# Performance work log

Hardware: AMD Instinct MI355X
Metric: run time of the kernel (lower is better)

## Reference

```python
import jax, jax.numpy as jnp
import numpy as np

TANH_CONST = 2.5
TEMPERATURE = 5.0


def setup_inputs() -> dict:
    key = jax.random.key(0)
    ks = jax.random.split(key, 9)
    B, L, NB, H, NC = 16384, 64, 8, 128, 1000
    return {
        "class_ids": jax.random.randint(ks[0], (B,), 0, NC),
        "gumbel_u": jax.random.uniform(ks[1], (L, B, NB), dtype=jnp.float32),
        "g_emb": jax.random.normal(ks[2], (NC, H), dtype=jnp.float32) * 0.1,
        "w_emb": jax.random.normal(ks[3], (NB, H), dtype=jnp.float32) * 0.1,
        "w_soft": jax.random.normal(ks[4], (NB, H), dtype=jnp.float32) * 0.1,
        "w_ih": jax.random.normal(ks[5], (4 * H, H), dtype=jnp.float32) * 0.1,
        "w_hh": jax.random.normal(ks[6], (4 * H, H), dtype=jnp.float32) * 0.1,
        "b_ih": jax.random.normal(ks[7], (4 * H,), dtype=jnp.float32) * 0.1,
        "b_hh": jax.random.normal(ks[8], (4 * H,), dtype=jnp.float32) * 0.1,
    }


def reference(class_ids, gumbel_u, g_emb, w_emb, w_soft, w_ih, w_hh, b_ih, b_hh):
    B = class_ids.shape[0]
    H = g_emb.shape[1]
    x0 = g_emb[class_ids]                      # [B, H] class embedding (reused each step)
    h0 = jnp.zeros((B, H), x0.dtype)
    c0 = jnp.zeros((B, H), x0.dtype)

    def step(carry, u):
        h, c, x = carry
        gates = x @ w_ih.T + h @ w_hh.T + b_ih + b_hh   # [B, 4H], torch gate order i,f,g,o
        i, f, g, o = jnp.split(gates, 4, axis=-1)
        c2 = jax.nn.sigmoid(f) * c + jax.nn.sigmoid(i) * jnp.tanh(g)
        h2 = jax.nn.sigmoid(o) * jnp.tanh(c2)
        logit = h2 @ w_soft.T                           # [B, NB]
        logit = TANH_CONST * jnp.tanh(logit / TEMPERATURE)
        # categorical sample via gumbel-max
        uc = jnp.clip(u, 1e-8, 1.0 - 1e-8)
        gmb = -jnp.log(-jnp.log(uc))
        branch = jnp.argmax(logit + gmb, axis=-1)       # [B] int
        logp = jax.nn.log_softmax(logit, axis=-1)
        lp = jnp.take_along_axis(logp, branch[:, None], axis=1)[:, 0]
        ent = -jnp.sum(jnp.exp(logp) * logp, axis=-1)
        x2 = (w_emb[branch] + x0) * 0.5
        return (h2, c2, x2), (branch, lp, ent)

    _, (arcs, lps, ents) = jax.lax.scan(step, (h0, c0, x0), gumbel_u)
    # stack along dim=1 like torch.stack(..., dim=1) -> [B, L]
    sample_arc = arcs.T
    sample_log_prob = lps.T
    sample_entropy = ents.T
    sample_prob = jnp.exp(sample_log_prob)
    return sample_arc, sample_log_prob, sample_entropy, sample_prob
```

## Files before the change

### kernel.cpp

```cpp
#include <hip/hip_runtime.h>
#include <math.h>

#define HD 128
#define NBR 8
#define LSTEPS 64
#define TILE_B 32
#define HT_PAD 36
#define PART_PAD 65

#define WHH2_OFF  0
#define WIH2_OFF  65536
#define PP_OFF    131072
#define BS_OFF    135168

__device__ __forceinline__ float fsig(float x) {
  return __builtin_amdgcn_rcpf(1.f + __expf(-x));
}
__device__ __forceinline__ float ftanh(float x) {
  return 1.f - 2.f * __builtin_amdgcn_rcpf(1.f + __expf(2.f * x));
}

__global__ __launch_bounds__(256) void setup_kernel(
    const float* __restrict__ w_emb, const float* __restrict__ w_ih,
    const float* __restrict__ w_hh, const float* __restrict__ b_ih,
    const float* __restrict__ b_hh, float* __restrict__ ws)
{
  int tid = blockIdx.x * blockDim.x + threadIdx.x;
  if (tid < 65536) {
    int hh = tid >> 9, k = (tid >> 2) & 127, q = tid & 3;
    ws[WHH2_OFF + tid] = w_hh[(q*HD + hh)*HD + k];
    ws[WIH2_OFF + tid] = w_ih[(q*HD + hh)*HD + k];
  }
  if (tid < 4096) {
    int j = tid >> 9, rem = tid & 511;
    int hh2 = rem >> 2, q = rem & 3;
    const float* wr = w_ih + (q*HD + hh2)*HD;
    const float* er = w_emb + j*HD;
    float s = 0.f;
    for (int k = 0; k < HD; ++k) s = fmaf(er[k], wr[k], s);
    ws[PP_OFF + tid] = 0.5f * s;
  }
  if (tid < 512) ws[BS_OFF + tid] = b_ih[tid] + b_hh[tid];
}

__global__ __launch_bounds__(256, 2) void ctrl_kernel(
    const int* __restrict__ class_ids,
    const float* __restrict__ gumbel_u,
    const float* __restrict__ g_emb,
    const float* __restrict__ w_soft,
    const float* __restrict__ ws,
    float* __restrict__ out,
    int Btot)
{
  __shared__ float hT[HD * HT_PAD];
  __shared__ float ws_l[NBR * HD];
  __shared__ float pp_l[NBR * HD * 4];
  __shared__ float part_l[TILE_B * PART_PAD];
  __shared__ int   br_l[TILE_B];

  const int tid = threadIdx.x;
  const int b0  = blockIdx.x * TILE_B;
  const size_t BL = (size_t)Btot * LSTEPS;

  for (int i = tid; i < NBR*HD; i += 256) ws_l[i] = w_soft[i];
  for (int i = tid; i < NBR*HD*4; i += 256) pp_l[i] = ws[PP_OFF + i];

  const int hh = tid & 127;
  const int bg = tid >> 7;

  float bsq[4];
  #pragma unroll
  for (int q = 0; q < 4; ++q) bsq[q] = ws[BS_OFF + q*HD + hh];

  const float* __restrict__ whhp = ws + WHH2_OFF + hh*512;
  const float* __restrict__ wihp = ws + WIH2_OFF + hh*512;
  const float* hTb = hT + bg*16;

  {
    int sb = tid >> 3;
    int kc = tid & 7;
    int cid = class_ids[b0 + sb];
    const float* src = g_emb + (size_t)cid * HD + kc*16;
    #pragma unroll
    for (int ii = 0; ii < 4; ++ii) {
      float4 v = *(const float4*)(src + 4*ii);
      int kb = kc*16 + 4*ii;
      hT[(kb+0)*HT_PAD + sb] = v.x;
      hT[(kb+1)*HT_PAD + sb] = v.y;
      hT[(kb+2)*HT_PAD + sb] = v.z;
      hT[(kb+3)*HT_PAD + sb] = v.w;
    }
  }
  __syncthreads();

  float q0[4][16];
  #pragma unroll
  for (int q = 0; q < 4; ++q)
    #pragma unroll
    for (int j = 0; j < 16; ++j) q0[q][j] = 0.f;

  #pragma unroll 8
  for (int k = 0; k < HD; ++k) {
    float4 w = *(const float4*)(wihp + k*4);
    const float* hr = hTb + k*HT_PAD;
    float4 h0 = *(const float4*)(hr);
    float4 h1 = *(const float4*)(hr+4);
    float4 h2 = *(const float4*)(hr+8);
    float4 h3 = *(const float4*)(hr+12);
    #pragma unroll
    for (int q = 0; q < 4; ++q) {
      float wq = (q==0)?w.x:((q==1)?w.y:((q==2)?w.z:w.w));
      q0[q][0]=fmaf(h0.x,wq,q0[q][0]); q0[q][1]=fmaf(h0.y,wq,q0[q][1]);
      q0[q][2]=fmaf(h0.z,wq,q0[q][2]); q0[q][3]=fmaf(h0.w,wq,q0[q][3]);
      q0[q][4]=fmaf(h1.x,wq,q0[q][4]); q0[q][5]=fmaf(h1.y,wq,q0[q][5]);
      q0[q][6]=fmaf(h1.z,wq,q0[q][6]); q0[q][7]=fmaf(h1.w,wq,q0[q][7]);
      q0[q][8]=fmaf(h2.x,wq,q0[q][8]); q0[q][9]=fmaf(h2.y,wq,q0[q][9]);
      q0[q][10]=fmaf(h2.z,wq,q0[q][10]); q0[q][11]=fmaf(h2.w,wq,q0[q][11]);
      q0[q][12]=fmaf(h3.x,wq,q0[q][12]); q0[q][13]=fmaf(h3.y,wq,q0[q][13]);
      q0[q][14]=fmaf(h3.z,wq,q0[q][14]); q0[q][15]=fmaf(h3.w,wq,q0[q][15]);
    }
  }
  __syncthreads();

  float c[16];
  #pragma unroll
  for (int j = 0; j < 16; ++j) c[j] = 0.f;

  for (int t = 0; t < LSTEPS; ++t) {
    float4 ua = make_float4(0,0,0,0), ub = make_float4(0,0,0,0);
    if (tid < TILE_B) {
      const float* up = gumbel_u + ((size_t)t * Btot + (b0 + tid)) * NBR;
      ua = *(const float4*)up;
      ub = *(const float4*)(up + 4);
    }

    float h2v[16];

    if (t == 0) {
      #pragma unroll
      for (int j = 0; j < 16; ++j) {
        float gi = q0[0][j] + bsq[0];
        float gf = q0[1][j] + bsq[1];
        float gg = q0[2][j] + bsq[2];
        float go = q0[3][j] + bsq[3];
        float c2 = fsig(gf)*c[j] + fsig(gi)*ftanh(gg);
        c[j] = c2;
        h2v[j] = fsig(go) * ftanh(c2);
      }
      #pragma unroll
      for (int q = 0; q < 4; ++q)
        #pragma unroll
        for (int j = 0; j < 16; ++j) q0[q][j] = fmaf(q0[q][j], 0.5f, bsq[q]);
    } else {
      float acc[4][16];
      #pragma unroll
      for (int q = 0; q < 4; ++q)
        #pragma unroll
        for (int j = 0; j < 16; ++j) acc[q][j] = 0.f;

      #pragma unroll 8
      for (int k = 0; k < HD; ++k) {
        float4 w = *(const float4*)(whhp + k*4);
        const float* hr = hTb + k*HT_PAD;
        float4 h0 = *(const float4*)(hr);
        float4 h1 = *(const float4*)(hr+4);
        float4 h2 = *(const float4*)(hr+8);
        float4 h3 = *(const float4*)(hr+12);
        #pragma unroll
        for (int q = 0; q < 4; ++q) {
          float wq = (q==0)?w.x:((q==1)?w.y:((q==2)?w.z:w.w));
          acc[q][0]=fmaf(h0.x,wq,acc[q][0]); acc[q][1]=fmaf(h0.y,wq,acc[q][1]);
          acc[q][2]=fmaf(h0.z,wq,acc[q][2]); acc[q][3]=fmaf(h0.w,wq,acc[q][3]);
          acc[q][4]=fmaf(h1.x,wq,acc[q][4]); acc[q][5]=fmaf(h1.y,wq,acc[q][5]);
          acc[q][6]=fmaf(h1.z,wq,acc[q][6]); acc[q][7]=fmaf(h1.w,wq,acc[q][7]);
          acc[q][8]=fmaf(h2.x,wq,acc[q][8]); acc[q][9]=fmaf(h2.y,wq,acc[q][9]);
          acc[q][10]=fmaf(h2.z,wq,acc[q][10]); acc[q][11]=fmaf(h2.w,wq,acc[q][11]);
          acc[q][12]=fmaf(h3.x,wq,acc[q][12]); acc[q][13]=fmaf(h3.y,wq,acc[q][13]);
          acc[q][14]=fmaf(h3.z,wq,acc[q][14]); acc[q][15]=fmaf(h3.w,wq,acc[q][15]);
        }
      }

      #pragma unroll
      for (int j = 0; j < 16; ++j) {
        int br = br_l[bg*16 + j];
        float4 pv = *(const float4*)(&pp_l[(br*HD + hh)*4]);
        float gi = (acc[0][j] + q0[0][j]) + pv.x;
        float gf = (acc[1][j] + q0[1][j]) + pv.y;
        float gg = (acc[2][j] + q0[2][j]) + pv.z;
        float go = (acc[3][j] + q0[3][j]) + pv.w;
        float c2 = fsig(gf)*c[j] + fsig(gi)*ftanh(gg);
        c[j] = c2;
        h2v[j] = fsig(go) * ftanh(c2);
      }
    }
    __syncthreads();

    {
      float* dst = &hT[hh*HT_PAD + bg*16];
      *(float4*)(dst)    = make_float4(h2v[0],h2v[1],h2v[2],h2v[3]);
      *(float4*)(dst+4)  = make_float4(h2v[4],h2v[5],h2v[6],h2v[7]);
      *(float4*)(dst+8)  = make_float4(h2v[8],h2v[9],h2v[10],h2v[11]);
      *(float4*)(dst+12) = make_float4(h2v[12],h2v[13],h2v[14],h2v[15]);
    }
    __syncthreads();

    {
      int lb = tid & 31, ch = tid >> 5;
      float part[8];
      #pragma unroll
      for (int nb = 0; nb < 8; ++nb) part[nb] = 0.f;
      #pragma unroll
      for (int i = 0; i < 16; ++i) {
        float hvv = hT[(ch*16 + i)*HT_PAD + lb];
        #pragma unroll
        for (int nb = 0; nb < 8; ++nb)
          part[nb] = fmaf(hvv, ws_l[nb*HD + ch*16 + i], part[nb]);
      }
      #pragma unroll
      for (int nb = 0; nb < 8; ++nb)
        part_l[lb*PART_PAD + nb*8 + ch] = part[nb];
    }
    __syncthreads();

    if (tid < TILE_B) {
      int lb = tid;
      float lg[8];
      #pragma unroll
      for (int nb = 0; nb < 8; ++nb) {
        float s = 0.f;
        #pragma unroll
        for (int ch = 0; ch < 8; ++ch) s += part_l[lb*PART_PAD + nb*8 + ch];
        lg[nb] = 2.5f * ftanh(s * 0.2f);
      }
      float uv[8] = {ua.x,ua.y,ua.z,ua.w,ub.x,ub.y,ub.z,ub.w};
      int br = 0; float best;
      {
        float uc = fminf(fmaxf(uv[0], 1e-8f), 0.99999999f);
        best = lg[0] - __logf(-__logf(uc));
      }
      #pragma unroll
      for (int nb = 1; nb < 8; ++nb) {
        float uc = fminf(fmaxf(uv[nb], 1e-8f), 0.99999999f);
        float y = lg[nb] - __logf(-__logf(uc));
        if (y > best) { best = y; br = nb; }
      }
      float m = lg[0];
      #pragma unroll
      for (int nb = 1; nb < 8; ++nb) m = fmaxf(m, lg[nb]);
      float se = 0.f;
      #pragma unroll
      for (int nb = 0; nb < 8; ++nb) se += __expf(lg[nb] - m);
      float lse = __logf(se);
      float lp = (lg[br] - m) - lse;
      float ent = 0.f;
      #pragma unroll
      for (int nb = 0; nb < 8; ++nb) {
        float lpi = (lg[nb] - m) - lse;
        ent -= __expf(lpi) * lpi;
      }
      size_t row = (size_t)(b0 + lb) * LSTEPS + t;
      out[row]        = (float)br;
      out[BL + row]   = lp;
      out[2*BL + row] = ent;
      out[3*BL + row] = __expf(lp);
      br_l[lb] = br;
    }
    __syncthreads();
  }
}

extern "C" void kernel_launch(void* const* d_in, const int* in_sizes, int n_in,
                              void* d_out, int out_size, void* d_ws, size_t ws_size,
                              hipStream_t stream) {
  const int*   class_ids = (const int*)d_in[0];
  const float* gumbel_u  = (const float*)d_in[1];
  const float* g_emb     = (const float*)d_in[2];
  const float* w_emb     = (const float*)d_in[3];
  const float* w_soft    = (const float*)d_in[4];
  const float* w_ih      = (const float*)d_in[5];
  const float* w_hh      = (const float*)d_in[6];
  const float* b_ih      = (const float*)d_in[7];
  const float* b_hh      = (const float*)d_in[8];
  float* out = (float*)d_out;
  float* ws  = (float*)d_ws;
  int B = in_sizes[0];

  hipLaunchKernelGGL(setup_kernel, dim3(256), dim3(256), 0, stream,
                     w_emb, w_ih, w_hh, b_ih, b_hh, ws);
  hipLaunchKernelGGL(ctrl_kernel, dim3(B / TILE_B), dim3(256), 0, stream,
                     class_ids, gumbel_u, g_emb, w_soft, ws, out, B);
}
```

Measured before the change: 2.225 ms.

## Precompute per-class input projections and restructure LSTM recurrence to 128-thread blocks

Adds a setup pass that computes the class-embedding input projection (plus bias) for every class, so the main kernel looks up a per-class row instead of running a per-block x0 GEMM. The recurrent GEMM is remapped so 128 threads each own 8 gate columns (two hidden units, all four gates) for 16 batch rows, with h written straight to shared memory. This removes one barrier and the extra register transpose, and the gate weights now come from global/L2 instead of LDS. The risk is heavier register pressure (16x8 accumulators), lower thread-level parallelism per block, and extra setup work proportional to the number of classes.

```diff
diff --git a/kernel.cpp b/kernel.cpp
--- a/kernel.cpp
+++ b/kernel.cpp
@@ -6,12 +6,12 @@
 #define LSTEPS 64
 #define TILE_B 32
 #define HT_PAD 36
-#define PART_PAD 65
-
-#define WHH2_OFF  0
-#define WIH2_OFF  65536
-#define PP_OFF    131072
-#define BS_OFF    135168
+#define PART_PAD 33
+
+#define QB_OFF   0
+#define WHH_OFF  524288
+#define PP_OFF   589824
+#define B2_OFF   593920
 
 __device__ __forceinline__ float fsig(float x) {
   return __builtin_amdgcn_rcpf(1.f + __expf(-x));
@@ -21,32 +21,54 @@
 }
 
 __global__ __launch_bounds__(256) void setup_kernel(
-    const float* __restrict__ w_emb, const float* __restrict__ w_ih,
-    const float* __restrict__ w_hh, const float* __restrict__ b_ih,
-    const float* __restrict__ b_hh, float* __restrict__ ws)
+    const float* __restrict__ g_emb, const float* __restrict__ w_emb,
+    const float* __restrict__ w_ih,  const float* __restrict__ w_hh,
+    const float* __restrict__ b_ih,  const float* __restrict__ b_hh,
+    float* __restrict__ ws, int NC)
 {
-  int tid = blockIdx.x * blockDim.x + threadIdx.x;
-  if (tid < 65536) {
-    int hh = tid >> 9, k = (tid >> 2) & 127, q = tid & 3;
-    ws[WHH2_OFF + tid] = w_hh[(q*HD + hh)*HD + k];
-    ws[WIH2_OFF + tid] = w_ih[(q*HD + hh)*HD + k];
-  }
-  if (tid < 4096) {
-    int j = tid >> 9, rem = tid & 511;
-    int hh2 = rem >> 2, q = rem & 3;
-    const float* wr = w_ih + (q*HD + hh2)*HD;
-    const float* er = w_emb + j*HD;
+  int tid = blockIdx.x * 256 + threadIdx.x;
+  int qbN = NC * 512;
+  if (tid < qbN) {
+    int cls = tid >> 9, col = tid & 511;
+    int cg = col >> 3, hid = (col >> 2) & 1, q = col & 3;
+    int row = q*HD + 2*cg + hid;
+    const float* er = g_emb + (size_t)cls * HD;
+    const float* wr = w_ih + (size_t)row * HD;
     float s = 0.f;
     for (int k = 0; k < HD; ++k) s = fmaf(er[k], wr[k], s);
-    ws[PP_OFF + tid] = 0.5f * s;
-  }
-  if (tid < 512) ws[BS_OFF + tid] = b_ih[tid] + b_hh[tid];
-}
-
-__global__ __launch_bounds__(256, 2) void ctrl_kernel(
+    ws[QB_OFF + tid] = 0.5f * s + b_ih[row] + b_hh[row];
+    return;
+  }
+  int t2 = tid - qbN;
+  if (t2 < 65536) {
+    int k = t2 >> 9, col = t2 & 511;
+    int cg = col >> 3, hid = (col >> 2) & 1, q = col & 3;
+    ws[WHH_OFF + t2] = w_hh[(q*HD + 2*cg + hid)*HD + k];
+    return;
+  }
+  int t3 = t2 - 65536;
+  if (t3 < 4096) {
+    int br = t3 >> 9, col = t3 & 511;
+    int cg = col >> 3, hid = (col >> 2) & 1, q = col & 3;
+    int row = q*HD + 2*cg + hid;
+    const float* er = w_emb + br*HD;
+    const float* wr = w_ih + (size_t)row * HD;
+    float s = 0.f;
+    for (int k = 0; k < HD; ++k) s = fmaf(er[k], wr[k], s);
+    ws[PP_OFF + t3] = 0.5f * s;
+    return;
+  }
+  int t4 = t3 - 4096;
+  if (t4 < 512) {
+    int cg = t4 >> 3, hid = (t4 >> 2) & 1, q = t4 & 3;
+    int row = q*HD + 2*cg + hid;
+    ws[B2_OFF + t4] = b_ih[row] + b_hh[row];
+  }
+}
+
+__global__ __launch_bounds__(128, 1) void ctrl_kernel(
     const int* __restrict__ class_ids,
     const float* __restrict__ gumbel_u,
-    const float* __restrict__ g_emb,
     const float* __restrict__ w_soft,
     const float* __restrict__ ws,
     float* __restrict__ out,
@@ -54,77 +76,41 @@
 {
   __shared__ float hT[HD * HT_PAD];
   __shared__ float ws_l[NBR * HD];
-  __shared__ float pp_l[NBR * HD * 4];
   __shared__ float part_l[TILE_B * PART_PAD];
   __shared__ int   br_l[TILE_B];
 
   const int tid = threadIdx.x;
+  const int cg  = tid & 63;
+  const int bg  = tid >> 6;
   const int b0  = blockIdx.x * TILE_B;
   const size_t BL = (size_t)Btot * LSTEPS;
 
-  for (int i = tid; i < NBR*HD; i += 256) ws_l[i] = w_soft[i];
-  for (int i = tid; i < NBR*HD*4; i += 256) pp_l[i] = ws[PP_OFF + i];
-
-  const int hh = tid & 127;
-  const int bg = tid >> 7;
-
-  float bsq[4];
+  for (int i = tid; i < NBR*HD; i += 128) ws_l[i] = w_soft[i];
+
+  const float* __restrict__ wkbase = ws + WHH_OFF + cg*8;
+  const float* __restrict__ qb     = ws + QB_OFF + cg*8;
+  const float* __restrict__ ppb    = ws + PP_OFF + cg*8;
+
+  float bias8[8];
+  {
+    const float* bp = ws + B2_OFF + cg*8;
+    float4 bA = *(const float4*)(bp);
+    float4 bB = *(const float4*)(bp + 4);
+    bias8[0]=bA.x; bias8[1]=bA.y; bias8[2]=bA.z; bias8[3]=bA.w;
+    bias8[4]=bB.x; bias8[5]=bB.y; bias8[6]=bB.z; bias8[7]=bB.w;
+  }
+
+  int cidq[16];
   #pragma unroll
-  for (int q = 0; q < 4; ++q) bsq[q] = ws[BS_OFF + q*HD + hh];
-
-  const float* __restrict__ whhp = ws + WHH2_OFF + hh*512;
-  const float* __restrict__ wihp = ws + WIH2_OFF + hh*512;
-  const float* hTb = hT + bg*16;
-
-  {
-    int sb = tid >> 3;
-    int kc = tid & 7;
-    int cid = class_ids[b0 + sb];
-    const float* src = g_emb + (size_t)cid * HD + kc*16;
-    #pragma unroll
-    for (int ii = 0; ii < 4; ++ii) {
-      float4 v = *(const float4*)(src + 4*ii);
-      int kb = kc*16 + 4*ii;
-      hT[(kb+0)*HT_PAD + sb] = v.x;
-      hT[(kb+1)*HT_PAD + sb] = v.y;
-      hT[(kb+2)*HT_PAD + sb] = v.z;
-      hT[(kb+3)*HT_PAD + sb] = v.w;
-    }
-  }
-  __syncthreads();
-
-  float q0[4][16];
+  for (int j = 0; j < 16; ++j)
+    cidq[j] = class_ids[b0 + bg*16 + j] << 9;
+
+  float cc[16][2];
   #pragma unroll
-  for (int q = 0; q < 4; ++q)
-    #pragma unroll
-    for (int j = 0; j < 16; ++j) q0[q][j] = 0.f;
-
-  #pragma unroll 8
-  for (int k = 0; k < HD; ++k) {
-    float4 w = *(const float4*)(wihp + k*4);
-    const float* hr = hTb + k*HT_PAD;
-    float4 h0 = *(const float4*)(hr);
-    float4 h1 = *(const float4*)(hr+4);
-    float4 h2 = *(const float4*)(hr+8);
-    float4 h3 = *(const float4*)(hr+12);
-    #pragma unroll
-    for (int q = 0; q < 4; ++q) {
-      float wq = (q==0)?w.x:((q==1)?w.y:((q==2)?w.z:w.w));
-      q0[q][0]=fmaf(h0.x,wq,q0[q][0]); q0[q][1]=fmaf(h0.y,wq,q0[q][1]);
-      q0[q][2]=fmaf(h0.z,wq,q0[q][2]); q0[q][3]=fmaf(h0.w,wq,q0[q][3]);
-      q0[q][4]=fmaf(h1.x,wq,q0[q][4]); q0[q][5]=fmaf(h1.y,wq,q0[q][5]);
-      q0[q][6]=fmaf(h1.z,wq,q0[q][6]); q0[q][7]=fmaf(h1.w,wq,q0[q][7]);
-      q0[q][8]=fmaf(h2.x,wq,q0[q][8]); q0[q][9]=fmaf(h2.y,wq,q0[q][9]);
-      q0[q][10]=fmaf(h2.z,wq,q0[q][10]); q0[q][11]=fmaf(h2.w,wq,q0[q][11]);
-      q0[q][12]=fmaf(h3.x,wq,q0[q][12]); q0[q][13]=fmaf(h3.y,wq,q0[q][13]);
-      q0[q][14]=fmaf(h3.z,wq,q0[q][14]); q0[q][15]=fmaf(h3.w,wq,q0[q][15]);
-    }
-  }
-  __syncthreads();
-
-  float c[16];
-  #pragma unroll
-  for (int j = 0; j < 16; ++j) c[j] = 0.f;
+  for (int j = 0; j < 16; ++j) { cc[j][0] = 0.f; cc[j][1] = 0.f; }
+
+  const int s_lb = tid & 31;
+  const int s_ch = tid >> 5;
 
   for (int t = 0; t < LSTEPS; ++t) {
     float4 ua = make_float4(0,0,0,0), ub = make_float4(0,0,0,0);
@@ -134,91 +120,96 @@
       ub = *(const float4*)(up + 4);
     }
 
-    float h2v[16];
-
-    if (t == 0) {
-      #pragma unroll
-      for (int j = 0; j < 16; ++j) {
-        float gi = q0[0][j] + bsq[0];
-        float gf = q0[1][j] + bsq[1];
-        float gg = q0[2][j] + bsq[2];
-        float go = q0[3][j] + bsq[3];
-        float c2 = fsig(gf)*c[j] + fsig(gi)*ftanh(gg);
-        c[j] = c2;
-        h2v[j] = fsig(go) * ftanh(c2);
-      }
-      #pragma unroll
-      for (int q = 0; q < 4; ++q)
+    float acc[16][8];
+    #pragma unroll
+    for (int j = 0; j < 16; ++j)
+      #pragma unroll
+      for (int g = 0; g < 8; ++g) acc[j][g] = 0.f;
+
+    if (t > 0) {
+      const float* wk = wkbase;
+      const float* hr = &hT[bg*16];
+      #pragma unroll 2
+      for (int k = 0; k < HD; ++k) {
+        float4 w0 = *(const float4*)(wk);
+        float4 w1 = *(const float4*)(wk + 4);
+        wk += 512;
+        float4 h0 = *(const float4*)(hr);
+        float4 h1 = *(const float4*)(hr + 4);
+        float4 h2 = *(const float4*)(hr + 8);
+        float4 h3 = *(const float4*)(hr + 12);
+        hr += HT_PAD;
+        #define FMAJ(j, hv) \
+          acc[j][0]=fmaf(hv,w0.x,acc[j][0]); acc[j][1]=fmaf(hv,w0.y,acc[j][1]); \
+          acc[j][2]=fmaf(hv,w0.z,acc[j][2]); acc[j][3]=fmaf(hv,w0.w,acc[j][3]); \
+          acc[j][4]=fmaf(hv,w1.x,acc[j][4]); acc[j][5]=fmaf(hv,w1.y,acc[j][5]); \
+          acc[j][6]=fmaf(hv,w1.z,acc[j][6]); acc[j][7]=fmaf(hv,w1.w,acc[j][7]);
+        FMAJ(0,  h0.x) FMAJ(1,  h0.y) FMAJ(2,  h0.z) FMAJ(3,  h0.w)
+        FMAJ(4,  h1.x) FMAJ(5,  h1.y) FMAJ(6,  h1.z) FMAJ(7,  h1.w)
+        FMAJ(8,  h2.x) FMAJ(9,  h2.y) FMAJ(10, h2.z) FMAJ(11, h2.w)
+        FMAJ(12, h3.x) FMAJ(13, h3.y) FMAJ(14, h3.z) FMAJ(15, h3.w)
+        #undef FMAJ
+      }
+    }
+    __syncthreads();
+
+    #pragma unroll
+    for (int j = 0; j < 16; ++j) {
+      int jb = bg*16 + j;
+      const float* qrow = qb + cidq[j];
+      float4 qv0 = *(const float4*)(qrow);
+      float4 qv1 = *(const float4*)(qrow + 4);
+      float4 pv0, pv1;
+      if (t == 0) {
+        pv0.x = qv0.x - bias8[0]; pv0.y = qv0.y - bias8[1];
+        pv0.z = qv0.z - bias8[2]; pv0.w = qv0.w - bias8[3];
+        pv1.x = qv1.x - bias8[4]; pv1.y = qv1.y - bias8[5];
+        pv1.z = qv1.z - bias8[6]; pv1.w = qv1.w - bias8[7];
+      } else {
+        const float* prow = ppb + (br_l[jb] << 9);
+        pv0 = *(const float4*)(prow);
+        pv1 = *(const float4*)(prow + 4);
+      }
+      float gi = acc[j][0] + qv0.x + pv0.x;
+      float gf = acc[j][1] + qv0.y + pv0.y;
+      float gc = acc[j][2] + qv0.z + pv0.z;
+      float go = acc[j][3] + qv0.w + pv0.w;
+      float c0 = fsig(gf)*cc[j][0] + fsig(gi)*ftanh(gc);
+      cc[j][0] = c0;
+      hT[(2*cg)*HT_PAD + jb] = fsig(go)*ftanh(c0);
+      gi = acc[j][4] + qv1.x + pv1.x;
+      gf = acc[j][5] + qv1.y + pv1.y;
+      gc = acc[j][6] + qv1.z + pv1.z;
+      go = acc[j][7] + qv1.w + pv1.w;
+      float c1 = fsig(gf)*cc[j][1] + fsig(gi)*ftanh(gc);
+      cc[j][1] = c1;
+      hT[(2*cg+1)*HT_PAD + jb] = fsig(go)*ftanh(c1);
+    }
+    __syncthreads();
+
+    {
+      const float* hcol = &hT[(s_ch*32)*HT_PAD + s_lb];
+      float part[8];
+      #pragma unroll
+      for (int nb = 0; nb < 8; ++nb) part[nb] = 0.f;
+      #pragma unroll
+      for (int ii = 0; ii < 32; ii += 4) {
+        float hv0 = hcol[(ii+0)*HT_PAD];
+        float hv1 = hcol[(ii+1)*HT_PAD];
+        float hv2 = hcol[(ii+2)*HT_PAD];
+        float hv3 = hcol[(ii+3)*HT_PAD];
         #pragma unroll
-        for (int j = 0; j < 16; ++j) q0[q][j] = fmaf(q0[q][j], 0.5f, bsq[q]);
-    } else {
-      float acc[4][16];
-      #pragma unroll
-      for (int q = 0; q < 4; ++q)
-        #pragma unroll
-        for (int j = 0; j < 16; ++j) acc[q][j] = 0.f;
-
-      #pragma unroll 8
-      for (int k = 0; k < HD; ++k) {
-        float4 w = *(const float4*)(whhp + k*4);
-        const float* hr = hTb + k*HT_PAD;
-        float4 h0 = *(const float4*)(hr);
-        float4 h1 = *(const float4*)(hr+4);
-        float4 h2 = *(const float4*)(hr+8);
-        float4 h3 = *(const float4*)(hr+12);
-        #pragma unroll
-        for (int q = 0; q < 4; ++q) {
-          float wq = (q==0)?w.x:((q==1)?w.y:((q==2)?w.z:w.w));
-          acc[q][0]=fmaf(h0.x,wq,acc[q][0]); acc[q][1]=fmaf(h0.y,wq,acc[q][1]);
-          acc[q][2]=fmaf(h0.z,wq,acc[q][2]); acc[q][3]=fmaf(h0.w,wq,acc[q][3]);
-          acc[q][4]=fmaf(h1.x,wq,acc[q][4]); acc[q][5]=fmaf(h1.y,wq,acc[q][5]);
-          acc[q][6]=fmaf(h1.z,wq,acc[q][6]); acc[q][7]=fmaf(h1.w,wq,acc[q][7]);
-          acc[q][8]=fmaf(h2.x,wq,acc[q][8]); acc[q][9]=fmaf(h2.y,wq,acc[q][9]);
-          acc[q][10]=fmaf(h2.z,wq,acc[q][10]); acc[q][11]=fmaf(h2.w,wq,acc[q][11]);
-          acc[q][12]=fmaf(h3.x,wq,acc[q][12]); acc[q][13]=fmaf(h3.y,wq,acc[q][13]);
-          acc[q][14]=fmaf(h3.z,wq,acc[q][14]); acc[q][15]=fmaf(h3.w,wq,acc[q][15]);
+        for (int nb = 0; nb < 8; ++nb) {
+          float4 wv = *(const float4*)(&ws_l[nb*HD + s_ch*32 + ii]);
+          part[nb] = fmaf(hv0, wv.x, part[nb]);
+          part[nb] = fmaf(hv1, wv.y, part[nb]);
+          part[nb] = fmaf(hv2, wv.z, part[nb]);
+          part[nb] = fmaf(hv3, wv.w, part[nb]);
         }
       }
-
-      #pragma unroll
-      for (int j = 0; j < 16; ++j) {
-        int br = br_l[bg*16 + j];
-        float4 pv = *(const float4*)(&pp_l[(br*HD + hh)*4]);
-        float gi = (acc[0][j] + q0[0][j]) + pv.x;
-        float gf = (acc[1][j] + q0[1][j]) + pv.y;
-        float gg = (acc[2][j] + q0[2][j]) + pv.z;
-        float go = (acc[3][j] + q0[3][j]) + pv.w;
-        float c2 = fsig(gf)*c[j] + fsig(gi)*ftanh(gg);
-        c[j] = c2;
-        h2v[j] = fsig(go) * ftanh(c2);
-      }
-    }
-    __syncthreads();
-
-    {
-      float* dst = &hT[hh*HT_PAD + bg*16];
-      *(float4*)(dst)    = make_float4(h2v[0],h2v[1],h2v[2],h2v[3]);
-      *(float4*)(dst+4)  = make_float4(h2v[4],h2v[5],h2v[6],h2v[7]);
-      *(float4*)(dst+8)  = make_float4(h2v[8],h2v[9],h2v[10],h2v[11]);
-      *(float4*)(dst+12) = make_float4(h2v[12],h2v[13],h2v[14],h2v[15]);
-    }
-    __syncthreads();
-
-    {
-      int lb = tid & 31, ch = tid >> 5;
-      float part[8];
-      #pragma unroll
-      for (int nb = 0; nb < 8; ++nb) part[nb] = 0.f;
-      #pragma unroll
-      for (int i = 0; i < 16; ++i) {
-        float hvv = hT[(ch*16 + i)*HT_PAD + lb];
-        #pragma unroll
-        for (int nb = 0; nb < 8; ++nb)
-          part[nb] = fmaf(hvv, ws_l[nb*HD + ch*16 + i], part[nb]);
-      }
       #pragma unroll
       for (int nb = 0; nb < 8; ++nb)
-        part_l[lb*PART_PAD + nb*8 + ch] = part[nb];
+        part_l[s_lb*PART_PAD + nb*4 + s_ch] = part[nb];
     }
     __syncthreads();
 
@@ -227,9 +218,8 @@
       float lg[8];
       #pragma unroll
       for (int nb = 0; nb < 8; ++nb) {
-        float s = 0.f;
-        #pragma unroll
-        for (int ch = 0; ch < 8; ++ch) s += part_l[lb*PART_PAD + nb*8 + ch];
+        const float* pr = &part_l[lb*PART_PAD + nb*4];
+        float s = (pr[0] + pr[1]) + (pr[2] + pr[3]);
         lg[nb] = 2.5f * ftanh(s * 0.2f);
       }
       float uv[8] = {ua.x,ua.y,ua.z,ua.w,ub.x,ub.y,ub.z,ub.w};
@@ -283,10 +273,13 @@
   const float* b_hh      = (const float*)d_in[8];
   float* out = (float*)d_out;
   float* ws  = (float*)d_ws;
-  int B = in_sizes[0];
-
-  hipLaunchKernelGGL(setup_kernel, dim3(256), dim3(256), 0, stream,
-                     w_emb, w_ih, w_hh, b_ih, b_hh, ws);
-  hipLaunchKernelGGL(ctrl_kernel, dim3(B / TILE_B), dim3(256), 0, stream,
-                     class_ids, gumbel_u, g_emb, w_soft, ws, out, B);
-}
+  int B  = in_sizes[0];
+  int NC = in_sizes[2] / HD;
+
+  int setup_items = NC*512 + 65536 + 4096 + 512;
+  int setup_grid  = (setup_items + 255) / 256;
+  hipLaunchKernelGGL(setup_kernel, dim3(setup_grid), dim3(256), 0, stream,
+                     g_emb, w_emb, w_ih, w_hh, b_ih, b_hh, ws, NC);
+  hipLaunchKernelGGL(ctrl_kernel, dim3(B / TILE_B), dim3(128), 0, stream,
+                     class_ids, gumbel_u, w_soft, ws, out, B);
+}
```

Result: slower. 2.590 ms (+16.4%).
